# Performance work log

Hardware: AMD Instinct MI355X
Metric: run time of the kernel (lower is better)

Reference implementation:

```python
import jax, jax.numpy as jnp
import numpy as np

B, C, H, W = 64, 3, 384, 384
P = 16                      # patch_size
E = 768                     # embed_dim
NH, NW = H // P, W // P     # 24, 24
N = NH * NW                 # 576 patches


def setup_inputs() -> dict:
    key = jax.random.key(0)
    k_x, k_y, k_xs, k_w, k_b = jax.random.split(key, 5)
    x = jax.random.normal(k_x, (B, C, H, W), dtype=jnp.float32)
    ys = jax.random.randint(k_y, (B, N), 0, W - P, dtype=jnp.int32)
    xs = jax.random.randint(k_xs, (B, N), 0, W - P, dtype=jnp.int32)
    # Conv2d(in_chans, embed_dim, kernel=P, stride=P) parameters
    w = jax.random.normal(k_w, (E, C, P, P), dtype=jnp.float32) * 0.02
    b = jax.random.normal(k_b, (E,), dtype=jnp.float32) * 0.02
    return {"x": x, "ys": ys, "xs": xs, "w": w, "b": b}


def _gather_patches(x, ys, xs):
    # x: [B,C,H,W]; ys/xs: [B,N] top-left corners -> patches [B,N,C,P,P]
    def one_img(img, ys_b, xs_b):
        def one_patch(y, x0):
            return jax.lax.dynamic_slice(img, (0, y, x0), (C, P, P))
        return jax.vmap(one_patch)(ys_b, xs_b)
    return jax.vmap(one_img)(x, ys, xs)


def reference(x, ys, xs, w, b):
    # patch_positions, as in the torch module
    patch_positions = jnp.stack([ys, xs], axis=-1)          # [B,N,2]
    patches = _gather_patches(x, ys, xs)                    # [B,N,C,P,P]
    # Restitched image fed to a stride-P conv == per-patch projection.
    # Conv windows exactly coincide with the restitched patches, so the
    # patch_embed is a single contraction per patch (same math, one pass).
    tokens = jnp.einsum('bncpq,ecpq->bne', patches, w) + b  # [B,N,E]
    return tokens, patch_positions
```

## Files before the change

kernel.cpp:

```cpp
#include <hip/hip_runtime.h>

#define B_    64
#define C_    3
#define H_    384
#define W_    384
#define P_    16
#define E_    768
#define N_    576
#define M_    (B_ * N_)
#define K_    (C_ * P_ * P_)

#define BM    128
#define BN    128
#define BK    32

typedef __attribute__((ext_vector_type(8))) short  short8;
typedef __attribute__((ext_vector_type(4))) float  f32x4;

__device__ __forceinline__ unsigned short f2bf(float f) {
    unsigned int u = __float_as_uint(f);
    u += 0x7FFFu + ((u >> 16) & 1u);
    return (unsigned short)(u >> 16);
}

__device__ __forceinline__ void gload_lds16(const void* g, void* l) {
    __builtin_amdgcn_global_load_lds(
        (const __attribute__((address_space(1))) unsigned int*)g,
        (__attribute__((address_space(3))) unsigned int*)l,
        16, 0, 0);
}

__global__ __launch_bounds__(256)
void gather_kernel(const float* __restrict__ x,
                   const int*   __restrict__ ys,
                   const int*   __restrict__ xs,
                   unsigned short* __restrict__ Abf)
{
    const unsigned g = blockIdx.x * 256 + threadIdx.x;
    const unsigned patch = g / 192u;
    const unsigned r  = g - patch * 192u;
    const unsigned c  = r >> 6;
    const unsigned r2 = r & 63u;
    const unsigned py = r2 >> 2;
    const unsigned q  = r2 & 3u;

    const unsigned bimg = patch / (unsigned)N_;
    const int y  = ys[patch];
    const int xx = xs[patch];

    const float* src = x + (size_t)bimg * (C_ * H_ * W_)
                         + (size_t)c * (H_ * W_)
                         + (size_t)(y + py) * W_ + xx + q * 4;

    uint2 pk;
    pk.x = (unsigned)f2bf(src[0]) | ((unsigned)f2bf(src[1]) << 16);
    pk.y = (unsigned)f2bf(src[2]) | ((unsigned)f2bf(src[3]) << 16);
    *(uint2*)(Abf + (size_t)g * 4) = pk;
}

__global__ __launch_bounds__(256)
void wconv_kernel(const float* __restrict__ w, unsigned short* __restrict__ Wb)
{
    const unsigned g = blockIdx.x * 256 + threadIdx.x;
    float4 f = ((const float4*)w)[g];
    uint2 pk;
    pk.x = (unsigned)f2bf(f.x) | ((unsigned)f2bf(f.y) << 16);
    pk.y = (unsigned)f2bf(f.z) | ((unsigned)f2bf(f.w) << 16);
    *(uint2*)(Wb + (size_t)g * 4) = pk;
}

__global__ void gemm_bf16(const unsigned short* __restrict__ A,
                          const unsigned short* __restrict__ Wb,
                          const float* __restrict__ bias,
                          float*       __restrict__ out)
{
    __shared__ unsigned short Asm[BM * BK];
    __shared__ unsigned short Bsm[BN * BK];

    const int t    = threadIdx.x;
    const int e0   = blockIdx.x * BN;
    const int m0   = blockIdx.y * BM;
    const int wave = t >> 6;
    const int lane = t & 63;

    const int srow = wave * 32 + (lane >> 2);
    const int scol = (lane & 3) * 8;
    const unsigned short* Ag = A  + (size_t)(m0 + srow) * K_ + scol;
    const unsigned short* Bg = Wb + (size_t)(e0 + srow) * K_ + scol;
    unsigned short* Al = &Asm[srow * BK + scol];
    unsigned short* Bl = &Bsm[srow * BK + scol];

    const int wr   = (wave >> 1) * 64;
    const int wc   = (wave & 1) * 64;
    const int lm   = lane & 15;
    const int quad = lane >> 4;

    f32x4 acc[4][4];
#pragma unroll
    for (int i = 0; i < 4; ++i)
#pragma unroll
        for (int j = 0; j < 4; ++j)
            acc[i][j] = (f32x4){0.f, 0.f, 0.f, 0.f};

#pragma unroll 1
    for (int it = 0; it < K_ / BK; ++it) {
        const unsigned short* ag = Ag + it * BK;
        const unsigned short* bg = Bg + it * BK;
        gload_lds16(ag,           Al);
        gload_lds16(ag + 16 * K_, Al + 16 * BK);
        gload_lds16(bg,           Bl);
        gload_lds16(bg + 16 * K_, Bl + 16 * BK);

        __syncthreads();

        short8 af[4], bfr[4];
#pragma unroll
        for (int i = 0; i < 4; ++i)
            af[i] = *(const short8*)&Asm[(wr + i * 16 + lm) * BK + quad * 8];
#pragma unroll
        for (int j = 0; j < 4; ++j)
            bfr[j] = *(const short8*)&Bsm[(wc + j * 16 + lm) * BK + quad * 8];

#pragma unroll
        for (int i = 0; i < 4; ++i)
#pragma unroll
            for (int j = 0; j < 4; ++j)
                acc[i][j] = __builtin_amdgcn_mfma_f32_16x16x32_bf16(af[i], bfr[j], acc[i][j], 0, 0, 0);

        __syncthreads();
    }

    float bv[4];
#pragma unroll
    for (int j = 0; j < 4; ++j) bv[j] = bias[e0 + wc + j * 16 + lm];

#pragma unroll
    for (int i = 0; i < 4; ++i) {
#pragma unroll
        for (int j = 0; j < 4; ++j) {
            const int eo = e0 + wc + j * 16 + lm;
#pragma unroll
            for (int r = 0; r < 4; ++r) {
                const int mo = m0 + wr + i * 16 + quad * 4 + r;
                out[(size_t)mo * E_ + eo] = acc[i][j][r] + bv[j];
            }
        }
    }
}

__global__ void pos_kernel(const int* __restrict__ ys, const int* __restrict__ xs,
                           float* __restrict__ outp)
{
    int i = blockIdx.x * blockDim.x + threadIdx.x;
    if (i < M_) {
        outp[2 * i]     = (float)ys[i];
        outp[2 * i + 1] = (float)xs[i];
    }
}

extern "C" void kernel_launch(void* const* d_in, const int* in_sizes, int n_in,
                              void* d_out, int out_size, void* d_ws, size_t ws_size,
                              hipStream_t stream)
{
    const float* x    = (const float*)d_in[0];
    const int*   ys   = (const int*)d_in[1];
    const int*   xs   = (const int*)d_in[2];
    const float* w    = (const float*)d_in[3];
    const float* bias = (const float*)d_in[4];
    float* out = (float*)d_out;

    unsigned short* Abf = (unsigned short*)d_ws;
    unsigned short* Wb  = Abf + (size_t)M_ * K_;

    gather_kernel<<<(M_ * 192) / 256, 256, 0, stream>>>(x, ys, xs, Abf);
    wconv_kernel<<<(E_ * K_ / 4) / 256, 256, 0, stream>>>(w, Wb);

    dim3 grid(E_ / BN, M_ / BM);
    gemm_bf16<<<grid, 256, 0, stream>>>(Abf, Wb, bias, out);

    float* outp = out + (size_t)M_ * E_;
    pos_kernel<<<(M_ + 255) / 256, 256, 0, stream>>>(ys, xs, outp);
}
```

Baseline: 280.0 us.

## Double BK to 64 and remap GEMM blocks to XCD-local tiles

Raises the K-tile from 32 to 64, halving the number of loop iterations and barrier pairs and issuing two MFMA sub-steps per LDS fill. It also switches to a 1D grid whose block index is remapped so each of the 8 XCDs handles a contiguous band of M tiles across all 6 E tiles, which is meant to improve L2 reuse of A rows. LDS use per block doubles and the loads still have no double buffering.

```diff
diff --git a/kernel.cpp b/kernel.cpp
--- a/kernel.cpp
+++ b/kernel.cpp
@@ -12,7 +12,7 @@
 
 #define BM    128
 #define BN    128
-#define BK    32
+#define BK    64
 
 typedef __attribute__((ext_vector_type(8))) short  short8;
 typedef __attribute__((ext_vector_type(4))) float  f32x4;
@@ -69,26 +69,33 @@
     *(uint2*)(Wb + (size_t)g * 4) = pk;
 }
 
-__global__ void gemm_bf16(const unsigned short* __restrict__ A,
-                          const unsigned short* __restrict__ Wb,
-                          const float* __restrict__ bias,
-                          float*       __restrict__ out)
+__global__ __launch_bounds__(256)
+void gemm_bf16(const unsigned short* __restrict__ A,
+               const unsigned short* __restrict__ Wb,
+               const float* __restrict__ bias,
+               float*       __restrict__ out)
 {
     __shared__ unsigned short Asm[BM * BK];
     __shared__ unsigned short Bsm[BN * BK];
 
     const int t    = threadIdx.x;
-    const int e0   = blockIdx.x * BN;
-    const int m0   = blockIdx.y * BM;
     const int wave = t >> 6;
     const int lane = t & 63;
 
-    const int srow = wave * 32 + (lane >> 2);
-    const int scol = (lane & 3) * 8;
-    const unsigned short* Ag = A  + (size_t)(m0 + srow) * K_ + scol;
-    const unsigned short* Bg = Wb + (size_t)(e0 + srow) * K_ + scol;
-    unsigned short* Al = &Asm[srow * BK + scol];
-    unsigned short* Bl = &Bsm[srow * BK + scol];
+    const int b   = blockIdx.x;
+    const int xcd = b & 7;
+    const int idx = b >> 3;
+    const int mt  = xcd * 36 + idx / 6;
+    const int et  = idx % 6;
+    const int m0  = mt * BM;
+    const int e0  = et * BN;
+
+    const int r8 = lane >> 3;
+    const int c8 = (lane & 7) * 8;
+    const unsigned short* Ag = A  + (size_t)(m0 + wave * 32 + r8) * K_ + c8;
+    const unsigned short* Bg = Wb + (size_t)(e0 + wave * 32 + r8) * K_ + c8;
+    unsigned short* Al = &Asm[(wave * 32 + r8) * BK + c8];
+    unsigned short* Bl = &Bsm[(wave * 32 + r8) * BK + c8];
 
     const int wr   = (wave >> 1) * 64;
     const int wc   = (wave & 1) * 64;
@@ -106,26 +113,29 @@
     for (int it = 0; it < K_ / BK; ++it) {
         const unsigned short* ag = Ag + it * BK;
         const unsigned short* bg = Bg + it * BK;
-        gload_lds16(ag,           Al);
-        gload_lds16(ag + 16 * K_, Al + 16 * BK);
-        gload_lds16(bg,           Bl);
-        gload_lds16(bg + 16 * K_, Bl + 16 * BK);
+#pragma unroll
+        for (int inst = 0; inst < 4; ++inst) {
+            gload_lds16(ag + (size_t)(inst * 8) * K_, Al + inst * 8 * BK);
+            gload_lds16(bg + (size_t)(inst * 8) * K_, Bl + inst * 8 * BK);
+        }
 
         __syncthreads();
 
-        short8 af[4], bfr[4];
 #pragma unroll
-        for (int i = 0; i < 4; ++i)
-            af[i] = *(const short8*)&Asm[(wr + i * 16 + lm) * BK + quad * 8];
+        for (int s = 0; s < 2; ++s) {
+            short8 af[4], bfr[4];
 #pragma unroll
-        for (int j = 0; j < 4; ++j)
-            bfr[j] = *(const short8*)&Bsm[(wc + j * 16 + lm) * BK + quad * 8];
-
-#pragma unroll
-        for (int i = 0; i < 4; ++i)
+            for (int i = 0; i < 4; ++i)
+                af[i] = *(const short8*)&Asm[(wr + i * 16 + lm) * BK + s * 32 + quad * 8];
 #pragma unroll
             for (int j = 0; j < 4; ++j)
-                acc[i][j] = __builtin_amdgcn_mfma_f32_16x16x32_bf16(af[i], bfr[j], acc[i][j], 0, 0, 0);
+                bfr[j] = *(const short8*)&Bsm[(wc + j * 16 + lm) * BK + s * 32 + quad * 8];
+#pragma unroll
+            for (int i = 0; i < 4; ++i)
+#pragma unroll
+                for (int j = 0; j < 4; ++j)
+                    acc[i][j] = __builtin_amdgcn_mfma_f32_16x16x32_bf16(af[i], bfr[j], acc[i][j], 0, 0, 0);
+        }
 
         __syncthreads();
     }
@@ -175,8 +185,7 @@
     gather_kernel<<<(M_ * 192) / 256, 256, 0, stream>>>(x, ys, xs, Abf);
     wconv_kernel<<<(E_ * K_ / 4) / 256, 256, 0, stream>>>(w, Wb);
 
-    dim3 grid(E_ / BN, M_ / BM);
-    gemm_bf16<<<grid, 256, 0, stream>>>(Abf, Wb, bias, out);
+    gemm_bf16<<<(M_ / BM) * (E_ / BN), 256, 0, stream>>>(Abf, Wb, bias, out);
 
     float* outp = out + (size_t)M_ * E_;
     pos_kernel<<<(M_ + 255) / 256, 256, 0, stream>>>(ys, xs, outp);
```

New measurement: 273.3 us. 2.4% less time.

## Widen GEMM tile to 128x256 with 8 waves and XCD-aware block mapping

Applied to the files above, without the earlier changes.

Doubles the GEMM N-tile to 256 and uses 512 threads (8 waves, each still computing a 64x64 sub-tile), so each A tile loaded from global memory is reused across twice as many output columns. The launch becomes a 1D grid whose block index is remapped so that the blocks on each XCD (assigned by b&7) cover a contiguous range of M tiles and all three E tiles, which is meant to improve L2 locality of A and B. The cost is more LDS per block and larger blocks, which may lower occupancy, and the remapping hardcodes the tile counts (288 M-tiles, 3 E-tiles).

```diff
diff --git a/kernel.cpp b/kernel.cpp
--- a/kernel.cpp
+++ b/kernel.cpp
@@ -11,7 +11,7 @@
 #define K_    (C_ * P_ * P_)
 
 #define BM    128
-#define BN    128
+#define BN    256
 #define BK    32
 
 typedef __attribute__((ext_vector_type(8))) short  short8;
@@ -69,29 +69,38 @@
     *(uint2*)(Wb + (size_t)g * 4) = pk;
 }
 
-__global__ void gemm_bf16(const unsigned short* __restrict__ A,
-                          const unsigned short* __restrict__ Wb,
-                          const float* __restrict__ bias,
-                          float*       __restrict__ out)
+__global__ __launch_bounds__(512, 4)
+void gemm_bf16(const unsigned short* __restrict__ A,
+               const unsigned short* __restrict__ Wb,
+               const float* __restrict__ bias,
+               float*       __restrict__ out)
 {
     __shared__ unsigned short Asm[BM * BK];
     __shared__ unsigned short Bsm[BN * BK];
 
     const int t    = threadIdx.x;
-    const int e0   = blockIdx.x * BN;
-    const int m0   = blockIdx.y * BM;
     const int wave = t >> 6;
     const int lane = t & 63;
 
-    const int srow = wave * 32 + (lane >> 2);
+    const int b   = blockIdx.x;
+    const int xcd = b & 7;
+    const int idx = b >> 3;
+    const int mt  = xcd * 36 + idx / 3;
+    const int et  = idx % 3;
+    const int m0  = mt * BM;
+    const int e0  = et * BN;
+
+    const int srow = wave * 16 + (lane >> 2);
     const int scol = (lane & 3) * 8;
     const unsigned short* Ag = A  + (size_t)(m0 + srow) * K_ + scol;
-    const unsigned short* Bg = Wb + (size_t)(e0 + srow) * K_ + scol;
-    unsigned short* Al = &Asm[srow * BK + scol];
-    unsigned short* Bl = &Bsm[srow * BK + scol];
+    const unsigned short* Bg0 = Wb + (size_t)(e0 + srow) * K_ + scol;
+    const unsigned short* Bg1 = Wb + (size_t)(e0 + 128 + srow) * K_ + scol;
+    unsigned short* Al  = &Asm[srow * BK + scol];
+    unsigned short* Bl0 = &Bsm[srow * BK + scol];
+    unsigned short* Bl1 = &Bsm[(128 + srow) * BK + scol];
 
-    const int wr   = (wave >> 1) * 64;
-    const int wc   = (wave & 1) * 64;
+    const int wr   = (wave >> 2) * 64;
+    const int wc   = (wave & 3) * 64;
     const int lm   = lane & 15;
     const int quad = lane >> 4;
 
@@ -104,12 +113,10 @@
 
 #pragma unroll 1
     for (int it = 0; it < K_ / BK; ++it) {
-        const unsigned short* ag = Ag + it * BK;
-        const unsigned short* bg = Bg + it * BK;
-        gload_lds16(ag,           Al);
-        gload_lds16(ag + 16 * K_, Al + 16 * BK);
-        gload_lds16(bg,           Bl);
-        gload_lds16(bg + 16 * K_, Bl + 16 * BK);
+        const int ko = it * BK;
+        gload_lds16(Ag  + ko, Al);
+        gload_lds16(Bg0 + ko, Bl0);
+        gload_lds16(Bg1 + ko, Bl1);
 
         __syncthreads();
 
@@ -175,8 +182,7 @@
     gather_kernel<<<(M_ * 192) / 256, 256, 0, stream>>>(x, ys, xs, Abf);
     wconv_kernel<<<(E_ * K_ / 4) / 256, 256, 0, stream>>>(w, Wb);
 
-    dim3 grid(E_ / BN, M_ / BM);
-    gemm_bf16<<<grid, 256, 0, stream>>>(Abf, Wb, bias, out);
+    gemm_bf16<<<(M_ / BM) * (E_ / BN), 512, 0, stream>>>(Abf, Wb, bias, out);
 
     float* outp = out + (size_t)M_ * E_;
     pos_kernel<<<(M_ + 255) / 256, 256, 0, stream>>>(ys, xs, outp);
```

New measurement: 273.3 us. 2.4% less time.
